# Kernel tuning notes

Measured on AMD Instinct MI355X. Metric: run time of the kernel, lower is better.

Reference implementation:

```python
import jax, jax.numpy as jnp
import numpy as np

N = 100000          # nodes
E = 1600000         # edges
NODE_DIM = 128
EDGE_DIM = 1
EMB = 16            # out_channels per head
H = 2               # heads
HID = 32
OUT = 2
NEG_SLOPE = 0.2


def gatv2_layer(x, src, dst, eattr, Wl, bl, Wr, br, We, att, bias):
    """PyG GATv2Conv: add self-loops (edge_attr fill='mean'), edge attention,
    segment softmax over target nodes, scatter-add aggregation, concat heads."""
    n = x.shape[0]
    heads, ch = att.shape
    # --- add self loops; self-loop edge_attr = mean of incoming edge_attr per node ---
    ones = jnp.ones((src.shape[0],), dtype=x.dtype)
    deg = jax.ops.segment_sum(ones, dst, num_segments=n)
    loop_attr = jax.ops.segment_sum(eattr, dst, num_segments=n) / jnp.maximum(deg, 1.0)[:, None]
    idx = jnp.arange(n, dtype=src.dtype)
    src2 = jnp.concatenate([src, idx])
    dst2 = jnp.concatenate([dst, idx])
    eattr2 = jnp.concatenate([eattr, loop_attr], axis=0)
    # --- linear projections ---
    xl = (x @ Wl + bl).reshape(n, heads, ch)   # source-side (lin_l)
    xr = (x @ Wr + br).reshape(n, heads, ch)   # target-side (lin_r)
    ef = (eattr2 @ We).reshape(-1, heads, ch)  # edge features (lin_edge, no bias)
    # --- per-edge attention logits (GATv2: LeakyReLU inside, then att dot) ---
    e = xl[src2] + xr[dst2] + ef               # [E2, H, C]
    e = jnp.where(e >= 0, e, NEG_SLOPE * e)
    logits = jnp.einsum('ehc,hc->eh', e, att)  # [E2, H]
    # --- segment softmax over edges sharing the same target node ---
    m = jax.ops.segment_max(logits, dst2, num_segments=n)      # [N, H]
    a = jnp.exp(logits - m[dst2])
    denom = jax.ops.segment_sum(a, dst2, num_segments=n)
    alpha = a / denom[dst2]                                    # [E2, H]
    # --- scatter-add weighted source messages ---
    msg = (alpha[:, :, None] * xl[src2]).reshape(-1, heads * ch)
    out = jax.ops.segment_sum(msg, dst2, num_segments=n)       # [N, H*C]
    return out + bias


def setup_inputs() -> dict:
    key = jax.random.key(0)
    ks = jax.random.split(key, 24)
    p = lambda k, s: (jax.random.normal(k, s, dtype=jnp.float32) * 0.1)
    HC = H * EMB
    return {
        'x': jax.random.normal(ks[0], (N, NODE_DIM), dtype=jnp.float32),
        'edge_index': jax.random.randint(ks[1], (2, E), 0, N, dtype=jnp.int32),
        'edge_attr': jax.random.normal(ks[2], (E, EDGE_DIM), dtype=jnp.float32),
        # layer 1
        'Wl1': p(ks[3], (NODE_DIM, HC)), 'bl1': p(ks[4], (HC,)),
        'Wr1': p(ks[5], (NODE_DIM, HC)), 'br1': p(ks[6], (HC,)),
        'We1': p(ks[7], (EDGE_DIM, HC)), 'att1': p(ks[8], (H, EMB)), 'b1': p(ks[9], (HC,)),
        # layer 2 (input dim = H*EMB)
        'Wl2': p(ks[10], (HC, HC)), 'bl2': p(ks[11], (HC,)),
        'Wr2': p(ks[12], (HC, HC)), 'br2': p(ks[13], (HC,)),
        'We2': p(ks[14], (EDGE_DIM, HC)), 'att2': p(ks[15], (H, EMB)), 'b2': p(ks[16], (HC,)),
        # decoder MLP
        'Wd1': p(ks[17], (HC, HID)), 'bd1': p(ks[18], (HID,)),
        'Wd2': p(ks[19], (HID, OUT)), 'bd2': p(ks[20], (OUT,)),
    }


def reference(x, edge_index, edge_attr,
              Wl1, bl1, Wr1, br1, We1, att1, b1,
              Wl2, bl2, Wr2, br2, We2, att2, b2,
              Wd1, bd1, Wd2, bd2):
    src, dst = edge_index[0], edge_index[1]
    h = gatv2_layer(x, src, dst, edge_attr, Wl1, bl1, Wr1, br1, We1, att1, b1)
    h = gatv2_layer(h, src, dst, edge_attr, Wl2, bl2, Wr2, br2, We2, att2, b2)
    h = jax.nn.relu(h @ Wd1 + bd1)
    return h @ Wd2 + bd2
```

## Files before the change

### kernel.cpp

```cpp
#include <hip/hip_runtime.h>
#include <hip/hip_fp16.h>
#include <math.h>


#define NN 100000
#define NE 1600000
#define SLOT 48
#define NEG_SLOPE 0.2f

__global__ void scatter_kernel(const int* __restrict__ src, const int* __restrict__ dst,
                               const float* __restrict__ eattr,
                               int* __restrict__ counts, unsigned* __restrict__ pay) {
    int e = blockIdx.x * blockDim.x + threadIdx.x;
    if (e >= NE) return;
    int d = dst[e];
    int pos = atomicAdd(counts + d, 1);
    if (pos < SLOT) {
        unsigned hb = __half_as_ushort(__float2half_rn(eattr[e]));
        pay[(size_t)d * SLOT + pos] = ((unsigned)src[e] << 15) | (hb >> 1);
    }
}

__device__ __forceinline__ float pk_ea(unsigned p) {
    return __half2float(__ushort_as_half((unsigned short)((p & 0x7FFFu) << 1)));
}
__device__ __forceinline__ float lrelu(float v) {
    return (v >= 0.f) ? v : NEG_SLOPE * v;
}

template <int K>
__global__ void proj_kernel(const float* __restrict__ x,
                            const float* __restrict__ Wl, const float* __restrict__ bl,
                            const float* __restrict__ Wr, const float* __restrict__ br,
                            __half* __restrict__ xl, float* __restrict__ xr) {
    __shared__ __align__(16) float sWl[K * 32];
    __shared__ __align__(16) float sWr[K * 32];
    __shared__ float sb[64];
    for (int i = threadIdx.x; i < K * 32; i += blockDim.x) {
        int k = i >> 5, col = i & 31;
        int p = (((k >> 2) ^ (col & 7)) << 2) | (k & 3);
        sWl[col * K + p] = Wl[i];
        sWr[col * K + p] = Wr[i];
    }
    if (threadIdx.x < 32) sb[threadIdx.x] = bl[threadIdx.x];
    else if (threadIdx.x < 64) sb[threadIdx.x] = br[threadIdx.x - 32];
    __syncthreads();
    int t = blockIdx.x * blockDim.x + threadIdx.x;
    int g = t >> 5, col = t & 31;
    int row0 = g * 4;
    if (row0 >= NN) return;
    const float4* x0 = (const float4*)(x + (size_t)(row0 + 0) * K);
    const float4* x1 = (const float4*)(x + (size_t)(row0 + 1) * K);
    const float4* x2 = (const float4*)(x + (size_t)(row0 + 2) * K);
    const float4* x3 = (const float4*)(x + (size_t)(row0 + 3) * K);
    const float4* wl4 = (const float4*)(sWl + col * K);
    const float4* wr4 = (const float4*)(sWr + col * K);
    int swz = col & 7;
    float al0 = 0.f, al1 = 0.f, al2 = 0.f, al3 = 0.f;
    float ar0 = 0.f, ar1 = 0.f, ar2 = 0.f, ar3 = 0.f;
#pragma unroll 4
    for (int k4 = 0; k4 < K / 4; k4++) {
        float4 wl = wl4[k4 ^ swz];
        float4 wr = wr4[k4 ^ swz];
        float4 a = x0[k4];
        float4 b = x1[k4];
        float4 c = x2[k4];
        float4 d = x3[k4];
        al0 = fmaf(a.x, wl.x, al0); al0 = fmaf(a.y, wl.y, al0);
        al0 = fmaf(a.z, wl.z, al0); al0 = fmaf(a.w, wl.w, al0);
        ar0 = fmaf(a.x, wr.x, ar0); ar0 = fmaf(a.y, wr.y, ar0);
        ar0 = fmaf(a.z, wr.z, ar0); ar0 = fmaf(a.w, wr.w, ar0);
        al1 = fmaf(b.x, wl.x, al1); al1 = fmaf(b.y, wl.y, al1);
        al1 = fmaf(b.z, wl.z, al1); al1 = fmaf(b.w, wl.w, al1);
        ar1 = fmaf(b.x, wr.x, ar1); ar1 = fmaf(b.y, wr.y, ar1);
        ar1 = fmaf(b.z, wr.z, ar1); ar1 = fmaf(b.w, wr.w, ar1);
        al2 = fmaf(c.x, wl.x, al2); al2 = fmaf(c.y, wl.y, al2);
        al2 = fmaf(c.z, wl.z, al2); al2 = fmaf(c.w, wl.w, al2);
        ar2 = fmaf(c.x, wr.x, ar2); ar2 = fmaf(c.y, wr.y, ar2);
        ar2 = fmaf(c.z, wr.z, ar2); ar2 = fmaf(c.w, wr.w, ar2);
        al3 = fmaf(d.x, wl.x, al3); al3 = fmaf(d.y, wl.y, al3);
        al3 = fmaf(d.z, wl.z, al3); al3 = fmaf(d.w, wl.w, al3);
        ar3 = fmaf(d.x, wr.x, ar3); ar3 = fmaf(d.y, wr.y, ar3);
        ar3 = fmaf(d.z, wr.z, ar3); ar3 = fmaf(d.w, wr.w, ar3);
    }
    float bls = sb[col], brs = sb[32 + col];
    xl[(size_t)(row0 + 0) * 32 + col] = __float2half_rn(al0 + bls);
    xr[(size_t)(row0 + 0) * 32 + col] = ar0 + brs;
    xl[(size_t)(row0 + 1) * 32 + col] = __float2half_rn(al1 + bls);
    xr[(size_t)(row0 + 1) * 32 + col] = ar1 + brs;
    xl[(size_t)(row0 + 2) * 32 + col] = __float2half_rn(al2 + bls);
    xr[(size_t)(row0 + 2) * 32 + col] = ar2 + brs;
    xl[(size_t)(row0 + 3) * 32 + col] = __float2half_rn(al3 + bls);
    xr[(size_t)(row0 + 3) * 32 + col] = ar3 + brs;
}

__device__ __forceinline__ void gat_core4(const int* __restrict__ counts,
                                          const unsigned* __restrict__ pay,
                                          const __half* xl, const float* xr,
                                          const float* We, const float* att,
                                          const float* bias, int node, int L,
                                          float h[4]) {
    int k = L & 7, j = L >> 3;
    int cnt = counts[node];
    int deg = (cnt < SLOT) ? cnt : SLOT;
    const unsigned* row = pay + (size_t)node * SLOT;
    float4 we = ((const float4*)We)[k];
    float4 at = ((const float4*)att)[k];
    float4 xrc = ((const float4*)(xr + (size_t)node * 32))[k];
    ushort4 sq = ((const ushort4*)(xl + (size_t)node * 32))[k];
    float sx0 = __half2float(__ushort_as_half(sq.x));
    float sx1 = __half2float(__ushort_as_half(sq.y));
    float sx2 = __half2float(__ushort_as_half(sq.z));
    float sx3 = __half2float(__ushort_as_half(sq.w));
    float ssum = 0.f, a0 = 0.f, a1 = 0.f, a2 = 0.f, a3 = 0.f, easum = 0.f;
    unsigned pv = row[j];
    for (int base = 0; base < deg; base += 4) {
        int idx = base + j;
        unsigned pvc = pv;
        int nidx = idx + 4;
        if (nidx > SLOT - 1) nidx = SLOT - 1;
        pv = row[nidx];
        bool valid = idx < deg;
        int s = valid ? (int)(pvc >> 15) : 0;
        float ea = pk_ea(pvc);
        ushort4 q = ((const ushort4*)(xl + (size_t)s * 32))[k];
        float x0 = __half2float(__ushort_as_half(q.x));
        float x1 = __half2float(__ushort_as_half(q.y));
        float x2 = __half2float(__ushort_as_half(q.z));
        float x3 = __half2float(__ushort_as_half(q.w));
        float p;
        p  = at.x * lrelu(fmaf(ea, we.x, x0 + xrc.x));
        p  = fmaf(at.y, lrelu(fmaf(ea, we.y, x1 + xrc.y)), p);
        p  = fmaf(at.z, lrelu(fmaf(ea, we.z, x2 + xrc.z)), p);
        p  = fmaf(at.w, lrelu(fmaf(ea, we.w, x3 + xrc.w)), p);
        p += __shfl_xor(p, 1);
        p += __shfl_xor(p, 2);
        float w = valid ? __expf(p) : 0.f;
        ssum += w;
        easum += valid ? ea : 0.f;
        a0 = fmaf(w, x0, a0);
        a1 = fmaf(w, x1, a1);
        a2 = fmaf(w, x2, a2);
        a3 = fmaf(w, x3, a3);
    }
    ssum  += __shfl_xor(ssum, 8);   ssum  += __shfl_xor(ssum, 16);
    easum += __shfl_xor(easum, 8);  easum += __shfl_xor(easum, 16);
    a0 += __shfl_xor(a0, 8);  a0 += __shfl_xor(a0, 16);
    a1 += __shfl_xor(a1, 8);  a1 += __shfl_xor(a1, 16);
    a2 += __shfl_xor(a2, 8);  a2 += __shfl_xor(a2, 16);
    a3 += __shfl_xor(a3, 8);  a3 += __shfl_xor(a3, 16);
    {
        float ea0 = easum / fmaxf((float)cnt, 1.f);
        float p;
        p  = at.x * lrelu(fmaf(ea0, we.x, sx0 + xrc.x));
        p  = fmaf(at.y, lrelu(fmaf(ea0, we.y, sx1 + xrc.y)), p);
        p  = fmaf(at.z, lrelu(fmaf(ea0, we.z, sx2 + xrc.z)), p);
        p  = fmaf(at.w, lrelu(fmaf(ea0, we.w, sx3 + xrc.w)), p);
        p += __shfl_xor(p, 1);
        p += __shfl_xor(p, 2);
        float w = __expf(p);
        ssum += w;
        a0 = fmaf(w, sx0, a0);
        a1 = fmaf(w, sx1, a1);
        a2 = fmaf(w, sx2, a2);
        a3 = fmaf(w, sx3, a3);
    }
    float4 bq = ((const float4*)bias)[k];
    float inv = 1.f / ssum;
    h[0] = a0 * inv + bq.x;
    h[1] = a1 * inv + bq.y;
    h[2] = a2 * inv + bq.z;
    h[3] = a3 * inv + bq.w;
}

__global__ void gat1_proj2_kernel(const int* __restrict__ counts,
                                  const unsigned* __restrict__ pay,
                                  const __half* __restrict__ xl, const float* __restrict__ xr,
                                  const float* __restrict__ We, const float* __restrict__ att,
                                  const float* __restrict__ bias,
                                  const float* __restrict__ Wl2, const float* __restrict__ bl2,
                                  const float* __restrict__ Wr2, const float* __restrict__ br2,
                                  __half* __restrict__ xl2, float* __restrict__ xr2) {
    __shared__ __align__(16) float sWl[1024];
    __shared__ __align__(16) float sWr[1024];
    __shared__ float4 hbuf[8][8];
    for (int i = threadIdx.x; i < 1024; i += blockDim.x) {
        int cc = i >> 5, Lc = i & 31;
        int p = (((cc >> 2) ^ (Lc & 7)) << 2) | (cc & 3);
        sWl[Lc * 32 + p] = Wl2[i];
        sWr[Lc * 32 + p] = Wr2[i];
    }
    __syncthreads();
    int t = blockIdx.x * blockDim.x + threadIdx.x;
    int node = t >> 5, L = t & 31;
    if (node >= NN) return;
    float h[4];
    gat_core4(counts, pay, xl, xr, We, att, bias, node, L, h);
    int nl = threadIdx.x >> 5;
    if (L < 8) hbuf[nl][L] = make_float4(h[0], h[1], h[2], h[3]);
    __syncthreads();
    const float4* hv4 = hbuf[nl];
    const float4* wl4 = (const float4*)(sWl + L * 32);
    const float4* wr4 = (const float4*)(sWr + L * 32);
    int swz = L & 7;
    float al = bl2[L], ar = br2[L];
#pragma unroll
    for (int c4 = 0; c4 < 8; c4++) {
        float4 hv = hv4[c4];
        float4 wl = wl4[c4 ^ swz];
        float4 wr = wr4[c4 ^ swz];
        al = fmaf(hv.x, wl.x, al); al = fmaf(hv.y, wl.y, al);
        al = fmaf(hv.z, wl.z, al); al = fmaf(hv.w, wl.w, al);
        ar = fmaf(hv.x, wr.x, ar); ar = fmaf(hv.y, wr.y, ar);
        ar = fmaf(hv.z, wr.z, ar); ar = fmaf(hv.w, wr.w, ar);
    }
    xl2[(size_t)node * 32 + L] = __float2half_rn(al);
    xr2[(size_t)node * 32 + L] = ar;
}

__global__ void gat2_dec_kernel(const int* __restrict__ counts,
                                const unsigned* __restrict__ pay,
                                const __half* __restrict__ xl, const float* __restrict__ xr,
                                const float* __restrict__ We, const float* __restrict__ att,
                                const float* __restrict__ bias,
                                const float* __restrict__ Wd1, const float* __restrict__ bd1,
                                const float* __restrict__ Wd2, const float* __restrict__ bd2,
                                float* __restrict__ out) {
    __shared__ __align__(16) float sWd1[1024];
    __shared__ float sWd2[64];
    __shared__ float4 hbuf[8][8];
    for (int i = threadIdx.x; i < 1024; i += blockDim.x) {
        int cc = i >> 5, Lc = i & 31;
        int p = (((cc >> 2) ^ (Lc & 7)) << 2) | (cc & 3);
        sWd1[Lc * 32 + p] = Wd1[i];
    }
    if (threadIdx.x < 64) sWd2[threadIdx.x] = Wd2[threadIdx.x];
    __syncthreads();
    int t = blockIdx.x * blockDim.x + threadIdx.x;
    int node = t >> 5, L = t & 31;
    if (node >= NN) return;
    float h[4];
    gat_core4(counts, pay, xl, xr, We, att, bias, node, L, h);
    int nl = threadIdx.x >> 5;
    if (L < 8) hbuf[nl][L] = make_float4(h[0], h[1], h[2], h[3]);
    __syncthreads();
    const float4* hv4 = hbuf[nl];
    const float4* wd4 = (const float4*)(sWd1 + L * 32);
    int swz = L & 7;
    float d1 = bd1[L];
#pragma unroll
    for (int c4 = 0; c4 < 8; c4++) {
        float4 hv = hv4[c4];
        float4 wd = wd4[c4 ^ swz];
        d1 = fmaf(hv.x, wd.x, d1); d1 = fmaf(hv.y, wd.y, d1);
        d1 = fmaf(hv.z, wd.z, d1); d1 = fmaf(hv.w, wd.w, d1);
    }
    float hid = fmaxf(d1, 0.f);
    float o0 = hid * sWd2[L * 2 + 0];
    float o1 = hid * sWd2[L * 2 + 1];
    o0 += __shfl_xor(o0, 1);   o1 += __shfl_xor(o1, 1);
    o0 += __shfl_xor(o0, 2);   o1 += __shfl_xor(o1, 2);
    o0 += __shfl_xor(o0, 4);   o1 += __shfl_xor(o1, 4);
    o0 += __shfl_xor(o0, 8);   o1 += __shfl_xor(o1, 8);
    o0 += __shfl_xor(o0, 16);  o1 += __shfl_xor(o1, 16);
    if (L == 0) {
        out[(size_t)node * 2 + 0] = o0 + bd2[0];
        out[(size_t)node * 2 + 1] = o1 + bd2[1];
    }
}

extern "C" void kernel_launch(void* const* d_in, const int* in_sizes, int n_in,
                              void* d_out, int out_size, void* d_ws, size_t ws_size,
                              hipStream_t stream) {
    const float* x     = (const float*)d_in[0];
    const int*   src   = (const int*)d_in[1];
    const int*   dst   = src + NE;
    const float* eattr = (const float*)d_in[2];
    const float* Wl1 = (const float*)d_in[3],  *bl1 = (const float*)d_in[4];
    const float* Wr1 = (const float*)d_in[5],  *br1 = (const float*)d_in[6];
    const float* We1 = (const float*)d_in[7],  *att1 = (const float*)d_in[8];
    const float* b1  = (const float*)d_in[9];
    const float* Wl2 = (const float*)d_in[10], *bl2 = (const float*)d_in[11];
    const float* Wr2 = (const float*)d_in[12], *br2 = (const float*)d_in[13];
    const float* We2 = (const float*)d_in[14], *att2 = (const float*)d_in[15];
    const float* b2  = (const float*)d_in[16];
    const float* Wd1 = (const float*)d_in[17], *bd1 = (const float*)d_in[18];
    const float* Wd2 = (const float*)d_in[19], *bd2 = (const float*)d_in[20];
    float* out = (float*)d_out;

    char* w = (char*)d_ws;
    int*      counts = (int*)w;       w += (size_t)NN * 4;
    unsigned* pay    = (unsigned*)w;  w += (size_t)NN * SLOT * 4;
    __half*   xl  = (__half*)w;       w += (size_t)NN * 32 * 2;
    float*    xr  = (float*)w;        w += (size_t)NN * 32 * 4;
    __half*   xl2 = (__half*)w;       w += (size_t)NN * 32 * 2;
    float*    xr2 = (float*)w;        w += (size_t)NN * 32 * 4;

    const int B = 256;
    const int gE   = NE / B;
    const int gN32 = (NN * 32) / B;
    const int gP   = (NN / 4 * 32) / B;

    hipMemsetAsync(counts, 0, (size_t)NN * 4, stream);
    scatter_kernel<<<gE, B, 0, stream>>>(src, dst, eattr, counts, pay);

    proj_kernel<128><<<gP, B, 0, stream>>>(x, Wl1, bl1, Wr1, br1, xl, xr);

    gat1_proj2_kernel<<<gN32, B, 0, stream>>>(counts, pay, xl, xr, We1, att1, b1,
                                              Wl2, bl2, Wr2, br2, xl2, xr2);

    gat2_dec_kernel<<<gN32, B, 0, stream>>>(counts, pay, xl2, xr2, We2, att2, b2,
                                            Wd1, bd1, Wd2, bd2, out);
}
```

Baseline: 415.3 us.

## Pad atomic counters, prefetch neighbor features a step ahead, replace block sync with wave fence

Spaces per-node edge counters 64 bytes apart so the atomics from the scatter pass land on separate cache lines and contend less. The gather loop now software-pipelines one extra stage, issuing the next neighbor's feature load and the payload load two steps ahead. It also replaces __syncthreads after the per-node shared buffer write with an LDS waitcnt plus scheduling barrier, since each 32-lane group only reads its own hbuf row. In exchange the counter array and its memset grow 16x and more registers are live in the loop. The fence relies on the writer and readers of each hbuf row sitting in the same wavefront.

```diff
diff --git a/kernel.cpp b/kernel.cpp
--- a/kernel.cpp
+++ b/kernel.cpp
@@ -6,6 +6,7 @@
 #define NN 100000
 #define NE 1600000
 #define SLOT 48
+#define CSTRIDE 16
 #define NEG_SLOPE 0.2f
 
 __global__ void scatter_kernel(const int* __restrict__ src, const int* __restrict__ dst,
@@ -14,7 +15,7 @@
     int e = blockIdx.x * blockDim.x + threadIdx.x;
     if (e >= NE) return;
     int d = dst[e];
-    int pos = atomicAdd(counts + d, 1);
+    int pos = atomicAdd(counts + (size_t)d * CSTRIDE, 1);
     if (pos < SLOT) {
         unsigned hb = __half_as_ushort(__float2half_rn(eattr[e]));
         pay[(size_t)d * SLOT + pos] = ((unsigned)src[e] << 15) | (hb >> 1);
@@ -101,7 +102,7 @@
                                           const float* bias, int node, int L,
                                           float h[4]) {
     int k = L & 7, j = L >> 3;
-    int cnt = counts[node];
+    int cnt = counts[(size_t)node * CSTRIDE];
     int deg = (cnt < SLOT) ? cnt : SLOT;
     const unsigned* row = pay + (size_t)node * SLOT;
     float4 we = ((const float4*)We)[k];
@@ -113,21 +114,24 @@
     float sx2 = __half2float(__ushort_as_half(sq.z));
     float sx3 = __half2float(__ushort_as_half(sq.w));
     float ssum = 0.f, a0 = 0.f, a1 = 0.f, a2 = 0.f, a3 = 0.f, easum = 0.f;
-    unsigned pv = row[j];
+    unsigned pv_c = row[j];
+    int n1 = j + 4; if (n1 > SLOT - 1) n1 = SLOT - 1;
+    unsigned pv_n = row[n1];
+    bool val_c = j < deg;
+    int s_c = val_c ? (int)(pv_c >> 15) : 0;
+    ushort4 q_c = ((const ushort4*)(xl + (size_t)s_c * 32))[k];
     for (int base = 0; base < deg; base += 4) {
         int idx = base + j;
-        unsigned pvc = pv;
-        int nidx = idx + 4;
-        if (nidx > SLOT - 1) nidx = SLOT - 1;
-        pv = row[nidx];
-        bool valid = idx < deg;
-        int s = valid ? (int)(pvc >> 15) : 0;
-        float ea = pk_ea(pvc);
-        ushort4 q = ((const ushort4*)(xl + (size_t)s * 32))[k];
-        float x0 = __half2float(__ushort_as_half(q.x));
-        float x1 = __half2float(__ushort_as_half(q.y));
-        float x2 = __half2float(__ushort_as_half(q.z));
-        float x3 = __half2float(__ushort_as_half(q.w));
+        bool val_n = (idx + 4) < deg;
+        int s_n = val_n ? (int)(pv_n >> 15) : 0;
+        ushort4 q_n = ((const ushort4*)(xl + (size_t)s_n * 32))[k];
+        int n2 = idx + 8; if (n2 > SLOT - 1) n2 = SLOT - 1;
+        unsigned pv_n2 = row[n2];
+        float ea = pk_ea(pv_c);
+        float x0 = __half2float(__ushort_as_half(q_c.x));
+        float x1 = __half2float(__ushort_as_half(q_c.y));
+        float x2 = __half2float(__ushort_as_half(q_c.z));
+        float x3 = __half2float(__ushort_as_half(q_c.w));
         float p;
         p  = at.x * lrelu(fmaf(ea, we.x, x0 + xrc.x));
         p  = fmaf(at.y, lrelu(fmaf(ea, we.y, x1 + xrc.y)), p);
@@ -135,13 +139,14 @@
         p  = fmaf(at.w, lrelu(fmaf(ea, we.w, x3 + xrc.w)), p);
         p += __shfl_xor(p, 1);
         p += __shfl_xor(p, 2);
-        float w = valid ? __expf(p) : 0.f;
+        float w = val_c ? __expf(p) : 0.f;
         ssum += w;
-        easum += valid ? ea : 0.f;
+        easum += val_c ? ea : 0.f;
         a0 = fmaf(w, x0, a0);
         a1 = fmaf(w, x1, a1);
         a2 = fmaf(w, x2, a2);
         a3 = fmaf(w, x3, a3);
+        pv_c = pv_n; pv_n = pv_n2; q_c = q_n; val_c = val_n;
     }
     ssum  += __shfl_xor(ssum, 8);   ssum  += __shfl_xor(ssum, 16);
     easum += __shfl_xor(easum, 8);  easum += __shfl_xor(easum, 16);
@@ -173,6 +178,11 @@
     h[3] = a3 * inv + bq.w;
 }
 
+#define HBUF_FENCE() do { \
+    asm volatile("s_waitcnt lgkmcnt(0)" ::: "memory"); \
+    __builtin_amdgcn_sched_barrier(0); \
+} while (0)
+
 __global__ void gat1_proj2_kernel(const int* __restrict__ counts,
                                   const unsigned* __restrict__ pay,
                                   const __half* __restrict__ xl, const float* __restrict__ xr,
@@ -198,7 +208,7 @@
     gat_core4(counts, pay, xl, xr, We, att, bias, node, L, h);
     int nl = threadIdx.x >> 5;
     if (L < 8) hbuf[nl][L] = make_float4(h[0], h[1], h[2], h[3]);
-    __syncthreads();
+    HBUF_FENCE();
     const float4* hv4 = hbuf[nl];
     const float4* wl4 = (const float4*)(sWl + L * 32);
     const float4* wr4 = (const float4*)(sWr + L * 32);
@@ -243,7 +253,7 @@
     gat_core4(counts, pay, xl, xr, We, att, bias, node, L, h);
     int nl = threadIdx.x >> 5;
     if (L < 8) hbuf[nl][L] = make_float4(h[0], h[1], h[2], h[3]);
-    __syncthreads();
+    HBUF_FENCE();
     const float4* hv4 = hbuf[nl];
     const float4* wd4 = (const float4*)(sWd1 + L * 32);
     int swz = L & 7;
@@ -289,7 +299,7 @@
     float* out = (float*)d_out;
 
     char* w = (char*)d_ws;
-    int*      counts = (int*)w;       w += (size_t)NN * 4;
+    int*      counts = (int*)w;       w += (size_t)NN * CSTRIDE * 4;
     unsigned* pay    = (unsigned*)w;  w += (size_t)NN * SLOT * 4;
     __half*   xl  = (__half*)w;       w += (size_t)NN * 32 * 2;
     float*    xr  = (float*)w;        w += (size_t)NN * 32 * 4;
@@ -301,7 +311,7 @@
     const int gN32 = (NN * 32) / B;
     const int gP   = (NN / 4 * 32) / B;
 
-    hipMemsetAsync(counts, 0, (size_t)NN * 4, stream);
+    hipMemsetAsync(counts, 0, (size_t)NN * CSTRIDE * 4, stream);
     scatter_kernel<<<gE, B, 0, stream>>>(src, dst, eattr, counts, pay);
 
     proj_kernel<128><<<gP, B, 0, stream>>>(x, Wl1, bl1, Wr1, br1, xl, xr);
```

Measured after the change: 409.4 us. About the same (-1.4%).
